# Kernel tuning notes

Measured on AMD Instinct MI355X. Metric: run time of the kernel, lower is better.

## Reference

```python
import jax, jax.numpy as jnp
import numpy as np

K = 3          # kernel_size
STRIDE = 1
PAD = 1
DIL = 1
K2 = K * K


def conv2d(x, w, b):
    # standard NCHW conv matching nn.Conv2d(stride, padding, dilation)
    y = jax.lax.conv_general_dilated(
        x, w, window_strides=(STRIDE, STRIDE),
        padding=[(PAD, PAD), (PAD, PAD)], rhs_dilation=(DIL, DIL),
        dimension_numbers=('NCHW', 'OIHW', 'NCHW'))
    return y + b[None, :, None, None]


def setup_inputs() -> dict:
    key = jax.random.key(0)
    ks = jax.random.split(key, 7)
    B, C, H, W, O = 4, 64, 128, 128, 64
    x = jax.random.normal(ks[0], (B, C, H, W), jnp.float32)
    weight = jax.random.normal(ks[1], (O, C, K, K), jnp.float32) * 0.05
    bias = jax.random.normal(ks[2], (O,), jnp.float32) * 0.05
    # offset/modulation convs (small weights so sample points stay near grid)
    offset_w = jax.random.normal(ks[3], (2 * K2, C, K, K), jnp.float32) * 0.01
    offset_b = jax.random.normal(ks[4], (2 * K2,), jnp.float32) * 0.1
    mod_w = jax.random.normal(ks[5], (K2, C, K, K), jnp.float32) * 0.01
    mod_b = jnp.ones((K2,), jnp.float32)  # torch init: modulation bias = 1
    return dict(x=x, weight=weight, bias=bias, offset_w=offset_w,
                offset_b=offset_b, mod_w=mod_w, mod_b=mod_b)


def _forward(x, weight, bias, offset_w, offset_b, mod_w, mod_b):
    B, C, H, W = x.shape
    O = weight.shape[0]
    offsets = conv2d(x, offset_w, offset_b)              # (B, 2*K2, Ho, Wo)
    mod = jax.nn.sigmoid(conv2d(x, mod_w, mod_b))        # (B, K2, Ho, Wo)
    Ho, Wo = offsets.shape[2], offsets.shape[3]
    off = offsets.reshape(B, 2, K2, Ho, Wo)
    # base sampling position: single center per output pixel (as in source)
    base_y = jnp.arange(Ho, dtype=x.dtype) * STRIDE - PAD + (K // 2) * DIL
    base_x = jnp.arange(Wo, dtype=x.dtype) * STRIDE - PAD + (K // 2) * DIL
    sy = base_y[None, None, :, None] + off[:, 0]         # (B, K2, Ho, Wo)
    sx = base_x[None, None, None, :] + off[:, 1]
    # bilinear sampling, zero padding, align_corners=True semantics
    y0 = jnp.floor(sy)
    x0 = jnp.floor(sx)
    wy1 = sy - y0
    wx1 = sx - x0
    y0i = y0.astype(jnp.int32)
    x0i = x0.astype(jnp.int32)
    P = K2 * Ho * Wo
    xf = x.reshape(B, C, H * W)

    def gather(yi, xi):
        valid = ((yi >= 0) & (yi < H) & (xi >= 0) & (xi < W))
        lin = (jnp.clip(yi, 0, H - 1) * W + jnp.clip(xi, 0, W - 1)).reshape(B, P)
        g = jax.vmap(lambda xb, lb: xb[:, lb])(xf, lin)   # (B, C, P)
        return g * valid.reshape(B, 1, P).astype(x.dtype)

    wy1f = wy1.reshape(B, 1, P)
    wx1f = wx1.reshape(B, 1, P)
    g00 = gather(y0i, x0i)
    g01 = gather(y0i, x0i + 1)
    g10 = gather(y0i + 1, x0i)
    g11 = gather(y0i + 1, x0i + 1)
    sampled = ((1.0 - wy1f) * ((1.0 - wx1f) * g00 + wx1f * g01)
               + wy1f * ((1.0 - wx1f) * g10 + wx1f * g11))
    sampled = sampled.reshape(B, C, K2, Ho * Wo)
    wk = weight.reshape(O, C, K2)
    out = jnp.einsum('bckp,ock->bop', sampled, wk).reshape(B, O, Ho, Wo)
    out = out * mod.mean(axis=1, keepdims=True) + bias[None, :, None, None]
    return out


def reference(x, weight, bias, offset_w, offset_b, mod_w, mod_b):
    return _forward(x, weight, bias, offset_w, offset_b, mod_w, mod_b)
```

## Files before the change

kernel.cpp:

```cpp
#include <hip/hip_runtime.h>
#include <math.h>

namespace {

constexpr int B = 4, C = 64, O = 64, H = 128, W = 128, K2 = 9;
constexpr int HW = H * W;
constexpr int PIX = 128;
constexpr int STR = 64;
constexpr int WROWS = 4, WCOLS = STR + 3, WCELLS = WROWS * WCOLS;

typedef __attribute__((ext_vector_type(8))) short short8v;
typedef __attribute__((ext_vector_type(4))) float f32x4;
typedef __attribute__((ext_vector_type(2))) float f32x2;
typedef __attribute__((ext_vector_type(4))) unsigned u32x4;

__device__ __forceinline__ unsigned f2bf(float f) {
    unsigned u = __float_as_uint(f);
    return (u + 0x7FFFu + ((u >> 16) & 1u)) >> 16;
}
__device__ __forceinline__ unsigned cvtpk(float lo, float hi) {
    unsigned r;
    asm("v_cvt_pk_bf16_f32 %0, %1, %2" : "=v"(r) : "v"(lo), "v"(hi));
    return r;
}
__device__ __forceinline__ f32x2 up2(unsigned d) {
    f32x2 r;
    r[0] = __uint_as_float(d << 16);
    r[1] = __uint_as_float(d & 0xffff0000u);
    return r;
}
__device__ __forceinline__ int swz(int r, int off) {
    return (r << 7) + (off ^ ((r & 7) << 4));
}

constexpr size_t WSW_OFF = 0;
constexpr size_t WSA_OFF = 73728;
constexpr size_t WS_NEED = 110592;

__global__ void k0_pack(const float* __restrict__ w, const float* __restrict__ ow,
                        const float* __restrict__ mw, unsigned char* __restrict__ ws)
{
    const int id = blockIdx.x * 256 + threadIdx.x;
    if (id < 4608) {
        const int k = id >> 9, rem = id & 511, ks = rem >> 8, r2 = rem & 255;
        const int ot = r2 >> 6, lane = r2 & 63;
        const int o = ot * 16 + (lane & 15), cb = ks * 32 + (lane >> 4) * 8;
        unsigned pk[4];
        #pragma unroll
        for (int e = 0; e < 4; ++e)
            pk[e] = f2bf(w[(o * C + cb + 2 * e) * 9 + k])
                  | (f2bf(w[(o * C + cb + 2 * e + 1) * 9 + k]) << 16);
        *(uint4*)(ws + WSW_OFF + (size_t)id * 16) = make_uint4(pk[0], pk[1], pk[2], pk[3]);
    } else if (id < 6912) {
        const int id2 = id - 4608;
        const int k = id2 >> 8, rem = id2 & 255, ks = rem >> 7, r2 = rem & 127;
        const int mt = r2 >> 6, lane = r2 & 63;
        const int r = mt * 16 + (lane & 15), cb = ks * 32 + (lane >> 4) * 8;
        unsigned pk[4];
        #pragma unroll
        for (int e = 0; e < 4; ++e) {
            float v0 = 0.f, v1 = 0.f;
            const int c0 = cb + 2 * e;
            if (r < 18)      { v0 = ow[(r * C + c0) * 9 + k];        v1 = ow[(r * C + c0 + 1) * 9 + k]; }
            else if (r < 27) { v0 = mw[((r - 18) * C + c0) * 9 + k]; v1 = mw[((r - 18) * C + c0 + 1) * 9 + k]; }
            pk[e] = f2bf(v0) | (f2bf(v1) << 16);
        }
        *(uint4*)(ws + WSA_OFF + (size_t)id2 * 16) = make_uint4(pk[0], pk[1], pk[2], pk[3]);
    }
}

__global__ __launch_bounds__(256, 3)
void dcn_fused14(const float* __restrict__ x, const float* __restrict__ bias,
                 const float* __restrict__ ob, const float* __restrict__ mb,
                 const unsigned char* __restrict__ ws, float* __restrict__ out)
{
    __shared__ __align__(16) unsigned char sW[WCELLS * 128];
    __shared__ float offL[18 * STR];

    const int tid = threadIdx.x;
    const int lane = tid & 63, wv = tid >> 6;
    const int lrow = lane & 15, lk = lane >> 4;

    const int raw = blockIdx.x;
    const int bid = (raw & 7) * 128 + (raw >> 3);
    const int b = bid >> 8;
    const int s = bid & 255;
    const int ho = s >> 1;
    const int wo0 = (s & 1) * STR;

    const float* __restrict__ xb = x + b * C * HW;

    for (int t = tid; t < 2 * WCELLS; t += 256) {
        const int cell = t >> 1, chalf = t & 1;
        const int row = cell / WCOLS, col = cell - row * WCOLS;
        const int y = ho - 1 + row, xg = wo0 - 2 + col;
        const bool v = (y >= 0) & (y < H) & (xg >= 0) & (xg < W);
        const float vf = v ? 1.f : 0.f;
        const float* __restrict__ xp = xb + (v ? (y * W + xg) : 0);
        #pragma unroll
        for (int q = 0; q < 4; ++q) {
            unsigned pk[4];
            #pragma unroll
            for (int e = 0; e < 4; ++e) {
                const int c0 = chalf * 32 + q * 8 + 2 * e;
                pk[e] = cvtpk(vf * xp[c0 * HW], vf * xp[(c0 + 1) * HW]);
            }
            *(uint4*)(sW + swz(cell, chalf * 64 + q * 16)) = make_uint4(pk[0], pk[1], pk[2], pk[3]);
        }
    }
    __syncthreads();

    f32x4 oacc[2];
    #pragma unroll
    for (int mt = 0; mt < 2; ++mt)
        #pragma unroll
        for (int j = 0; j < 4; ++j) oacc[mt][j] = 0.f;

    #pragma unroll
    for (int k = 0; k < 9; ++k) {
        const int ky = k / 3, kx = k - ky * 3;
        const int cellb = ky * WCOLS + (wv * 16 + lrow) + kx + 1;
        #pragma unroll
        for (int ks = 0; ks < 2; ++ks) {
            short8v bf = *(const short8v*)(sW + swz(cellb, ks * 64 + lk * 16));
            #pragma unroll
            for (int mt = 0; mt < 2; ++mt) {
                short8v af = *(const short8v*)(ws + WSA_OFF +
                    (size_t)((((k * 2 + ks) * 2 + mt) * 64 + lane)) * 16);
                oacc[mt] = __builtin_amdgcn_mfma_f32_16x16x32_bf16(af, bf, oacc[mt], 0, 0, 0);
            }
        }
    }

    float mpart = 0.f;
    {
        const int pc = wv * 16 + lrow;
        #pragma unroll
        for (int mt = 0; mt < 2; ++mt) {
            #pragma unroll
            for (int j = 0; j < 4; ++j) {
                const int r = mt * 16 + lk * 4 + j;
                const float val = oacc[mt][j];
                if (r < 9)       offL[r * STR + pc] = (float)ho + ob[r] + val;
                else if (r < 18) offL[r * STR + pc] = (float)(wo0 + pc) + ob[r] + val;
                else if (r < 27) mpart += 1.f / (1.f + __expf(-(val + mb[r - 18])));
            }
        }
    }
    mpart += __shfl_xor(mpart, 16);
    mpart += __shfl_xor(mpart, 32);
    const float mm = mpart * (1.f / 9.f);
    __syncthreads();

    const int px = wv * 16 + lrow;

    float syr[9], sxr[9];
    #pragma unroll
    for (int k = 0; k < 9; ++k) {
        syr[k] = offL[k * STR + px];
        sxr[k] = offL[(9 + k) * STR + px];
    }

    f32x4 acc[4];
    #pragma unroll
    for (int ot = 0; ot < 4; ++ot)
        #pragma unroll
        for (int j = 0; j < 4; ++j) acc[ot][j] = 0.f;

    short8v afq[8], afn[8];
    #pragma unroll
    for (int i = 0; i < 8; ++i)
        afq[i] = *(const short8v*)(ws + WSW_OFF + (size_t)(i * 64 + lane) * 16);

    #pragma unroll
    for (int k = 0; k < 9; ++k) {
        const float syv = syr[k];
        const float sxv = sxr[k];
        const float fy = floorf(syv), fx = floorf(sxv);
        const float wy1 = syv - fy, wx1 = sxv - fx;
        const float wy0 = 1.f - wy1, wx0 = 1.f - wx1;
        const int y0 = (int)fy, x0 = (int)fx;
        const int rw = y0 - (ho - 1), cw = x0 - (wo0 - 2);
        const bool inw = (rw >= 0) & (rw <= WROWS - 2) & (cw >= 0) & (cw <= WCOLS - 2);
        const float u00 = wy0 * wx0, u01 = wy0 * wx1;
        const float u10 = wy1 * wx0, u11 = wy1 * wx1;

        short8v bfrag[2];
        if (__builtin_expect(inw, 1)) {
            const int c00 = rw * WCOLS + cw;
            #pragma unroll
            for (int ks = 0; ks < 2; ++ks) {
                const int chOff = ks * 64 + lk * 16;
                const uint4 d00 = *(const uint4*)(sW + swz(c00,             chOff));
                const uint4 d01 = *(const uint4*)(sW + swz(c00 + 1,         chOff));
                const uint4 d10 = *(const uint4*)(sW + swz(c00 + WCOLS,     chOff));
                const uint4 d11 = *(const uint4*)(sW + swz(c00 + WCOLS + 1, chOff));
                auto bil = [&](unsigned a, unsigned bb, unsigned c, unsigned d) -> unsigned {
                    f32x2 sacc = up2(a);
                    sacc *= u00;
                    sacc += up2(bb) * u01;
                    sacc += up2(c)  * u10;
                    sacc += up2(d)  * u11;
                    return cvtpk(sacc[0], sacc[1]);
                };
                u32x4 wvv;
                wvv[0] = bil(d00.x, d01.x, d10.x, d11.x);
                wvv[1] = bil(d00.y, d01.y, d10.y, d11.y);
                wvv[2] = bil(d00.z, d01.z, d10.z, d11.z);
                wvv[3] = bil(d00.w, d01.w, d10.w, d11.w);
                bfrag[ks] = __builtin_bit_cast(short8v, wvv);
            }
        } else {
            const float vy0 = (y0 >= 0 && y0 < H) ? 1.f : 0.f;
            const float vy1 = (y0 + 1 >= 0 && y0 + 1 < H) ? 1.f : 0.f;
            const float vx0 = (x0 >= 0 && x0 < W) ? 1.f : 0.f;
            const float vx1 = (x0 + 1 >= 0 && x0 + 1 < W) ? 1.f : 0.f;
            const int cy0 = min(max(y0, 0), H - 1), cy1 = min(max(y0 + 1, 0), H - 1);
            const int cx0 = min(max(x0, 0), W - 1), cx1 = min(max(x0 + 1, 0), W - 1);
            const int l00 = cy0 * W + cx0, l01 = cy0 * W + cx1;
            const int l10 = cy1 * W + cx0, l11 = cy1 * W + cx1;
            const float g00 = u00 * vy0 * vx0, g01 = u01 * vy0 * vx1;
            const float g10 = u10 * vy1 * vx0, g11 = u11 * vy1 * vx1;
            #pragma unroll
            for (int ks = 0; ks < 2; ++ks) {
                #pragma unroll
                for (int j = 0; j < 8; ++j) {
                    const float* __restrict__ xc = xb + (ks * 32 + lk * 8 + j) * HW;
                    const float sv = g00 * xc[l00] + g01 * xc[l01]
                                   + g10 * xc[l10] + g11 * xc[l11];
                    bfrag[ks][j] = (short)f2bf(sv);
                }
            }
        }

        if (k < 8) {
            #pragma unroll
            for (int i = 0; i < 8; ++i)
                afn[i] = *(const short8v*)(ws + WSW_OFF +
                    (size_t)(((k + 1) * 8 + i) * 64 + lane) * 16);
        }

        #pragma unroll
        for (int i = 0; i < 8; ++i)
            acc[i & 3] = __builtin_amdgcn_mfma_f32_16x16x32_bf16(
                afq[i], bfrag[i >> 2], acc[i & 3], 0, 0, 0);

        if (k < 8) {
            #pragma unroll
            for (int i = 0; i < 8; ++i) afq[i] = afn[i];
        }
    }

    #pragma unroll
    for (int ot = 0; ot < 4; ++ot) {
        #pragma unroll
        for (int j = 0; j < 4; ++j) {
            const int o = ot * 16 + lk * 4 + j;
            out[(b * O + o) * HW + ho * W + wo0 + px] = acc[ot][j] * mm + bias[o];
        }
    }
}

__global__ __launch_bounds__(256, 2)
void dcn_fallback(const float* __restrict__ x, const float* __restrict__ weight,
                  const float* __restrict__ bias, const float* __restrict__ ow,
                  const float* __restrict__ ob, const float* __restrict__ mw,
                  const float* __restrict__ mb, float* __restrict__ out)
{
    __shared__ __align__(16) unsigned char sT[PIX * 128];
    __shared__ float offL[32 * PIX];
    __shared__ float mmL[PIX];

    const int tid = threadIdx.x;
    const int lane = tid & 63;
    const int wv = tid >> 6;
    const int bid = (blockIdx.x & 7) * 64 + (blockIdx.x >> 3);
    const int b = bid >> 7;
    const int ho = bid & 127;
    const float* __restrict__ xb = x + (size_t)b * C * HW;
    const int p = tid & 127, half = tid >> 7, wo = p;
    const int lrow = lane & 15, lk = lane >> 4;

    f32x4 oacc[2][2];
    #pragma unroll
    for (int mt = 0; mt < 2; ++mt)
        #pragma unroll
        for (int nt = 0; nt < 2; ++nt)
            #pragma unroll
            for (int j = 0; j < 4; ++j) oacc[mt][nt][j] = 0.0f;

    #pragma unroll
    for (int k = 0; k < K2; ++k) {
        const int ky = k / 3, kx = k % 3;
        short8v afrA[2][2];
        #pragma unroll
        for (int ks = 0; ks < 2; ++ks)
            #pragma unroll
            for (int mt = 0; mt < 2; ++mt) {
                const int r = mt * 16 + lrow, cb = ks * 32 + lk * 8;
                #pragma unroll
                for (int j = 0; j < 8; ++j) {
                    float wvv = 0.0f;
                    if (r < 18)      wvv = ow[((size_t)(r * C + cb + j)) * 9 + k];
                    else if (r < 27) wvv = mw[((size_t)((r - 18) * C + cb + j)) * 9 + k];
                    afrA[ks][mt][j] = (short)f2bf(wvv);
                }
            }
        {
            const int y = ho - 1 + ky, xx = wo - 1 + kx;
            const bool v = (y >= 0) & (y < H) & (xx >= 0) & (xx < W);
            const float vf = v ? 1.0f : 0.0f;
            const float* __restrict__ xp = xb + (v ? (y * W + xx) : 0);
            #pragma unroll
            for (int q = 0; q < 4; ++q) {
                unsigned pk[4];
                #pragma unroll
                for (int e = 0; e < 4; ++e) {
                    const int c0 = half * 32 + q * 8 + e * 2;
                    pk[e] = f2bf(vf * xp[(size_t)c0 * HW]) | (f2bf(vf * xp[(size_t)(c0 + 1) * HW]) << 16);
                }
                *(uint4*)(sT + swz(p, half * 64 + q * 16)) = make_uint4(pk[0], pk[1], pk[2], pk[3]);
            }
        }
        __syncthreads();
        #pragma unroll
        for (int ks = 0; ks < 2; ++ks)
            #pragma unroll
            for (int nt = 0; nt < 2; ++nt) {
                const int pc = wv * 32 + nt * 16 + lrow;
                short8v bfr = *(const short8v*)(sT + swz(pc, ks * 64 + lk * 16));
                #pragma unroll
                for (int mt = 0; mt < 2; ++mt)
                    oacc[mt][nt] = __builtin_amdgcn_mfma_f32_16x16x32_bf16(afrA[ks][mt], bfr, oacc[mt][nt], 0, 0, 0);
            }
        __syncthreads();
    }

    #pragma unroll
    for (int mt = 0; mt < 2; ++mt)
        #pragma unroll
        for (int nt = 0; nt < 2; ++nt)
            #pragma unroll
            for (int j = 0; j < 4; ++j) {
                const int r = mt * 16 + lk * 4 + j;
                const int pc = wv * 32 + nt * 16 + lrow;
                float bv = 0.0f;
                if (r < 18)      bv = ob[r];
                else if (r < 27) bv = mb[r - 18];
                offL[r * PIX + pc] = oacc[mt][nt][j] + bv;
            }
    __syncthreads();

    float sy[K2], sx[K2];
    #pragma unroll
    for (int k = 0; k < K2; ++k) {
        sy[k] = (float)ho + offL[k * PIX + p];
        sx[k] = (float)wo + offL[(9 + k) * PIX + p];
    }
    if (half == 0) {
        float mm = 0.0f;
        #pragma unroll
        for (int k = 0; k < K2; ++k)
            mm += 1.0f / (1.0f + __expf(-offL[(18 + k) * PIX + p]));
        mmL[p] = mm * (1.0f / 9.0f);
    }

    f32x4 acc[8];
    #pragma unroll
    for (int nt = 0; nt < 8; ++nt)
        #pragma unroll
        for (int j = 0; j < 4; ++j) acc[nt][j] = 0.0f;

    #pragma unroll
    for (int k = 0; k < K2; ++k) {
        short8v afr[2];
        #pragma unroll
        for (int ks = 0; ks < 2; ++ks) {
            const int o = wv * 16 + lrow, cb = ks * 32 + lk * 8;
            #pragma unroll
            for (int j = 0; j < 8; ++j)
                afr[ks][j] = (short)f2bf(weight[((size_t)(o * C + cb + j)) * 9 + k]);
        }
        {
            const float fy = floorf(sy[k]), fx = floorf(sx[k]);
            const float wy1 = sy[k] - fy, wx1 = sx[k] - fx;
            const float wy0 = 1.0f - wy1, wx0 = 1.0f - wx1;
            const int y0 = (int)fy, x0 = (int)fx, y1 = y0 + 1, x1 = x0 + 1;
            const float vy0 = (y0 >= 0 && y0 < H) ? 1.0f : 0.0f;
            const float vy1 = (y1 >= 0 && y1 < H) ? 1.0f : 0.0f;
            const float vx0 = (x0 >= 0 && x0 < W) ? 1.0f : 0.0f;
            const float vx1 = (x1 >= 0 && x1 < W) ? 1.0f : 0.0f;
            const int cy0 = min(max(y0, 0), H - 1), cy1 = min(max(y1, 0), H - 1);
            const int cx0 = min(max(x0, 0), W - 1), cx1 = min(max(x1, 0), W - 1);
            const int l00 = cy0 * W + cx0, l01 = cy0 * W + cx1;
            const int l10 = cy1 * W + cx0, l11 = cy1 * W + cx1;
            const float w00 = wy0 * wx0 * vy0 * vx0, w01 = wy0 * wx1 * vy0 * vx1;
            const float w10 = wy1 * wx0 * vy1 * vx0, w11 = wy1 * wx1 * vy1 * vx1;
            #pragma unroll
            for (int q = 0; q < 4; ++q) {
                unsigned pk[4];
                #pragma unroll
                for (int e = 0; e < 4; ++e) {
                    const int c0 = half * 32 + q * 8 + e * 2;
                    const float* __restrict__ xc0 = xb + (size_t)c0 * HW;
                    const float* __restrict__ xc1 = xc0 + HW;
                    const float s0 = w00 * xc0[l00] + w01 * xc0[l01] + w10 * xc0[l10] + w11 * xc0[l11];
                    const float s1 = w00 * xc1[l00] + w01 * xc1[l01] + w10 * xc1[l10] + w11 * xc1[l11];
                    pk[e] = f2bf(s0) | (f2bf(s1) << 16);
                }
                *(uint4*)(sT + swz(p, half * 64 + q * 16)) = make_uint4(pk[0], pk[1], pk[2], pk[3]);
            }
        }
        __syncthreads();
        #pragma unroll
        for (int ks = 0; ks < 2; ++ks)
            #pragma unroll
            for (int nt = 0; nt < 8; ++nt) {
                const int pc = nt * 16 + lrow;
                short8v bfr = *(const short8v*)(sT + swz(pc, ks * 64 + lk * 16));
                acc[nt] = __builtin_amdgcn_mfma_f32_16x16x32_bf16(afr[ks], bfr, acc[nt], 0, 0, 0);
            }
        __syncthreads();
    }

    float bv[4];
    #pragma unroll
    for (int j = 0; j < 4; ++j) bv[j] = bias[wv * 16 + lk * 4 + j];
    #pragma unroll
    for (int nt = 0; nt < 8; ++nt) {
        const int pc = nt * 16 + lrow;
        const float mmv = mmL[pc];
        #pragma unroll
        for (int j = 0; j < 4; ++j) {
            const int o = wv * 16 + lk * 4 + j;
            out[((size_t)(b * O + o)) * HW + ho * W + pc] = acc[nt][j] * mmv + bv[j];
        }
    }
}

}

extern "C" void kernel_launch(void* const* d_in, const int* in_sizes, int n_in,
                              void* d_out, int out_size, void* d_ws, size_t ws_size,
                              hipStream_t stream)
{
    const float* x  = (const float*)d_in[0];
    const float* w  = (const float*)d_in[1];
    const float* bs = (const float*)d_in[2];
    const float* ow = (const float*)d_in[3];
    const float* ob = (const float*)d_in[4];
    const float* mw = (const float*)d_in[5];
    const float* mb = (const float*)d_in[6];
    float* out = (float*)d_out;

    if (ws_size < WS_NEED) {
        dim3 grid(B * H), block(256);
        hipLaunchKernelGGL(dcn_fallback, grid, block, 0, stream,
                           x, w, bs, ow, ob, mw, mb, out);
        return;
    }

    unsigned char* ws = (unsigned char*)d_ws;
    hipLaunchKernelGGL(k0_pack, dim3(27), dim3(256), 0, stream, w, ow, mw, ws);
    hipLaunchKernelGGL(dcn_fused14, dim3(1024), dim3(256), 0, stream,
                       x, bs, ob, mb, (const unsigned char*)ws, out);
}
```

Baseline: 41.11 us.

## Process two output rows per block to share input window and weight fragments

Each block now covers two output rows instead of one. It loads a 5-row input window into LDS and reuses the main-conv weight fragments for both rows, then launches half as many blocks. The intent is to cut redundant global reads of the input halo and of the weights. In exchange it doubles the accumulator registers per thread and uses more LDS, which may lower occupancy under the 3-blocks-per-SIMD launch bound. With 512 blocks the grid gives the chip fewer waves to schedule.

```diff
diff --git a/kernel.cpp b/kernel.cpp
--- a/kernel.cpp
+++ b/kernel.cpp
@@ -7,7 +7,7 @@
 constexpr int HW = H * W;
 constexpr int PIX = 128;
 constexpr int STR = 64;
-constexpr int WROWS = 4, WCOLS = STR + 3, WCELLS = WROWS * WCOLS;
+constexpr int WROWS = 5, WCOLS = STR + 3, WCELLS = WROWS * WCOLS;
 
 typedef __attribute__((ext_vector_type(8))) short short8v;
 typedef __attribute__((ext_vector_type(4))) float f32x4;
@@ -70,30 +70,30 @@
 }
 
 __global__ __launch_bounds__(256, 3)
-void dcn_fused14(const float* __restrict__ x, const float* __restrict__ bias,
+void dcn_fused15(const float* __restrict__ x, const float* __restrict__ bias,
                  const float* __restrict__ ob, const float* __restrict__ mb,
                  const unsigned char* __restrict__ ws, float* __restrict__ out)
 {
     __shared__ __align__(16) unsigned char sW[WCELLS * 128];
-    __shared__ float offL[18 * STR];
+    __shared__ float offL[2 * 18 * STR];
 
     const int tid = threadIdx.x;
     const int lane = tid & 63, wv = tid >> 6;
     const int lrow = lane & 15, lk = lane >> 4;
 
     const int raw = blockIdx.x;
-    const int bid = (raw & 7) * 128 + (raw >> 3);
-    const int b = bid >> 8;
-    const int s = bid & 255;
-    const int ho = s >> 1;
-    const int wo0 = (s & 1) * STR;
+    const int bid = (raw & 7) * 64 + (raw >> 3);
+    const int b = bid >> 7;
+    const int r2_ = bid & 127;
+    const int ho0 = (r2_ >> 1) << 1;
+    const int wo0 = (r2_ & 1) << 6;
 
     const float* __restrict__ xb = x + b * C * HW;
 
     for (int t = tid; t < 2 * WCELLS; t += 256) {
         const int cell = t >> 1, chalf = t & 1;
         const int row = cell / WCOLS, col = cell - row * WCOLS;
-        const int y = ho - 1 + row, xg = wo0 - 2 + col;
+        const int y = ho0 - 1 + row, xg = wo0 - 2 + col;
         const bool v = (y >= 0) & (y < H) & (xg >= 0) & (xg < W);
         const float vf = v ? 1.f : 0.f;
         const float* __restrict__ xp = xb + (v ? (y * W + xg) : 0);
@@ -110,62 +110,61 @@
     }
     __syncthreads();
 
-    f32x4 oacc[2];
-    #pragma unroll
-    for (int mt = 0; mt < 2; ++mt)
-        #pragma unroll
-        for (int j = 0; j < 4; ++j) oacc[mt][j] = 0.f;
-
-    #pragma unroll
-    for (int k = 0; k < 9; ++k) {
-        const int ky = k / 3, kx = k - ky * 3;
-        const int cellb = ky * WCOLS + (wv * 16 + lrow) + kx + 1;
-        #pragma unroll
-        for (int ks = 0; ks < 2; ++ks) {
-            short8v bf = *(const short8v*)(sW + swz(cellb, ks * 64 + lk * 16));
+    float mmr[2];
+    #pragma unroll
+    for (int rr = 0; rr < 2; ++rr) {
+        f32x4 oacc[2];
+        #pragma unroll
+        for (int mt = 0; mt < 2; ++mt)
+            #pragma unroll
+            for (int j = 0; j < 4; ++j) oacc[mt][j] = 0.f;
+
+        #pragma unroll
+        for (int k = 0; k < 9; ++k) {
+            const int ky = k / 3, kx = k - ky * 3;
+            const int cellb = (rr + ky) * WCOLS + (wv * 16 + lrow) + kx + 1;
+            #pragma unroll
+            for (int ks = 0; ks < 2; ++ks) {
+                short8v bf = *(const short8v*)(sW + swz(cellb, ks * 64 + lk * 16));
+                #pragma unroll
+                for (int mt = 0; mt < 2; ++mt) {
+                    short8v af = *(const short8v*)(ws + WSA_OFF +
+                        (size_t)((((k * 2 + ks) * 2 + mt) * 64 + lane)) * 16);
+                    oacc[mt] = __builtin_amdgcn_mfma_f32_16x16x32_bf16(af, bf, oacc[mt], 0, 0, 0);
+                }
+            }
+        }
+
+        float mpart = 0.f;
+        {
+            const int pc = wv * 16 + lrow;
             #pragma unroll
             for (int mt = 0; mt < 2; ++mt) {
-                short8v af = *(const short8v*)(ws + WSA_OFF +
-                    (size_t)((((k * 2 + ks) * 2 + mt) * 64 + lane)) * 16);
-                oacc[mt] = __builtin_amdgcn_mfma_f32_16x16x32_bf16(af, bf, oacc[mt], 0, 0, 0);
-            }
-        }
-    }
-
-    float mpart = 0.f;
-    {
-        const int pc = wv * 16 + lrow;
-        #pragma unroll
-        for (int mt = 0; mt < 2; ++mt) {
-            #pragma unroll
-            for (int j = 0; j < 4; ++j) {
-                const int r = mt * 16 + lk * 4 + j;
-                const float val = oacc[mt][j];
-                if (r < 9)       offL[r * STR + pc] = (float)ho + ob[r] + val;
-                else if (r < 18) offL[r * STR + pc] = (float)(wo0 + pc) + ob[r] + val;
-                else if (r < 27) mpart += 1.f / (1.f + __expf(-(val + mb[r - 18])));
-            }
-        }
-    }
-    mpart += __shfl_xor(mpart, 16);
-    mpart += __shfl_xor(mpart, 32);
-    const float mm = mpart * (1.f / 9.f);
+                #pragma unroll
+                for (int j = 0; j < 4; ++j) {
+                    const int r = mt * 16 + lk * 4 + j;
+                    const float val = oacc[mt][j];
+                    if (r < 9)       offL[(rr * 18 + r) * STR + pc] = (float)(ho0 + rr) + ob[r] + val;
+                    else if (r < 18) offL[(rr * 18 + r) * STR + pc] = (float)(wo0 + pc) + ob[r] + val;
+                    else if (r < 27) mpart += 1.f / (1.f + __expf(-(val + mb[r - 18])));
+                }
+            }
+        }
+        mpart += __shfl_xor(mpart, 16);
+        mpart += __shfl_xor(mpart, 32);
+        mmr[rr] = mpart * (1.f / 9.f);
+    }
     __syncthreads();
 
     const int px = wv * 16 + lrow;
 
-    float syr[9], sxr[9];
-    #pragma unroll
-    for (int k = 0; k < 9; ++k) {
-        syr[k] = offL[k * STR + px];
-        sxr[k] = offL[(9 + k) * STR + px];
-    }
-
-    f32x4 acc[4];
-    #pragma unroll
-    for (int ot = 0; ot < 4; ++ot)
-        #pragma unroll
-        for (int j = 0; j < 4; ++j) acc[ot][j] = 0.f;
+    f32x4 acc[2][4];
+    #pragma unroll
+    for (int rr = 0; rr < 2; ++rr)
+        #pragma unroll
+        for (int ot = 0; ot < 4; ++ot)
+            #pragma unroll
+            for (int j = 0; j < 4; ++j) acc[rr][ot][j] = 0.f;
 
     short8v afq[8], afn[8];
     #pragma unroll
@@ -174,65 +173,6 @@
 
     #pragma unroll
     for (int k = 0; k < 9; ++k) {
-        const float syv = syr[k];
-        const float sxv = sxr[k];
-        const float fy = floorf(syv), fx = floorf(sxv);
-        const float wy1 = syv - fy, wx1 = sxv - fx;
-        const float wy0 = 1.f - wy1, wx0 = 1.f - wx1;
-        const int y0 = (int)fy, x0 = (int)fx;
-        const int rw = y0 - (ho - 1), cw = x0 - (wo0 - 2);
-        const bool inw = (rw >= 0) & (rw <= WROWS - 2) & (cw >= 0) & (cw <= WCOLS - 2);
-        const float u00 = wy0 * wx0, u01 = wy0 * wx1;
-        const float u10 = wy1 * wx0, u11 = wy1 * wx1;
-
-        short8v bfrag[2];
-        if (__builtin_expect(inw, 1)) {
-            const int c00 = rw * WCOLS + cw;
-            #pragma unroll
-            for (int ks = 0; ks < 2; ++ks) {
-                const int chOff = ks * 64 + lk * 16;
-                const uint4 d00 = *(const uint4*)(sW + swz(c00,             chOff));
-                const uint4 d01 = *(const uint4*)(sW + swz(c00 + 1,         chOff));
-                const uint4 d10 = *(const uint4*)(sW + swz(c00 + WCOLS,     chOff));
-                const uint4 d11 = *(const uint4*)(sW + swz(c00 + WCOLS + 1, chOff));
-                auto bil = [&](unsigned a, unsigned bb, unsigned c, unsigned d) -> unsigned {
-                    f32x2 sacc = up2(a);
-                    sacc *= u00;
-                    sacc += up2(bb) * u01;
-                    sacc += up2(c)  * u10;
-                    sacc += up2(d)  * u11;
-                    return cvtpk(sacc[0], sacc[1]);
-                };
-                u32x4 wvv;
-                wvv[0] = bil(d00.x, d01.x, d10.x, d11.x);
-                wvv[1] = bil(d00.y, d01.y, d10.y, d11.y);
-                wvv[2] = bil(d00.z, d01.z, d10.z, d11.z);
-                wvv[3] = bil(d00.w, d01.w, d10.w, d11.w);
-                bfrag[ks] = __builtin_bit_cast(short8v, wvv);
-            }
-        } else {
-            const float vy0 = (y0 >= 0 && y0 < H) ? 1.f : 0.f;
-            const float vy1 = (y0 + 1 >= 0 && y0 + 1 < H) ? 1.f : 0.f;
-            const float vx0 = (x0 >= 0 && x0 < W) ? 1.f : 0.f;
-            const float vx1 = (x0 + 1 >= 0 && x0 + 1 < W) ? 1.f : 0.f;
-            const int cy0 = min(max(y0, 0), H - 1), cy1 = min(max(y0 + 1, 0), H - 1);
-            const int cx0 = min(max(x0, 0), W - 1), cx1 = min(max(x0 + 1, 0), W - 1);
-            const int l00 = cy0 * W + cx0, l01 = cy0 * W + cx1;
-            const int l10 = cy1 * W + cx0, l11 = cy1 * W + cx1;
-            const float g00 = u00 * vy0 * vx0, g01 = u01 * vy0 * vx1;
-            const float g10 = u10 * vy1 * vx0, g11 = u11 * vy1 * vx1;
-            #pragma unroll
-            for (int ks = 0; ks < 2; ++ks) {
-                #pragma unroll
-                for (int j = 0; j < 8; ++j) {
-                    const float* __restrict__ xc = xb + (ks * 32 + lk * 8 + j) * HW;
-                    const float sv = g00 * xc[l00] + g01 * xc[l01]
-                                   + g10 * xc[l10] + g11 * xc[l11];
-                    bfrag[ks][j] = (short)f2bf(sv);
-                }
-            }
-        }
-
         if (k < 8) {
             #pragma unroll
             for (int i = 0; i < 8; ++i)
@@ -241,9 +181,71 @@
         }
 
         #pragma unroll
-        for (int i = 0; i < 8; ++i)
-            acc[i & 3] = __builtin_amdgcn_mfma_f32_16x16x32_bf16(
-                afq[i], bfrag[i >> 2], acc[i & 3], 0, 0, 0);
+        for (int rr = 0; rr < 2; ++rr) {
+            const float syv = offL[(rr * 18 + k) * STR + px];
+            const float sxv = offL[(rr * 18 + 9 + k) * STR + px];
+            const float fy = floorf(syv), fx = floorf(sxv);
+            const float wy1 = syv - fy, wx1 = sxv - fx;
+            const float wy0 = 1.f - wy1, wx0 = 1.f - wx1;
+            const int y0 = (int)fy, x0 = (int)fx;
+            const int wrow = y0 - (ho0 - 1), cw = x0 - (wo0 - 2);
+            const bool inw = (wrow >= 0) & (wrow <= WROWS - 2) & (cw >= 0) & (cw <= WCOLS - 2);
+            const float u00 = wy0 * wx0, u01 = wy0 * wx1;
+            const float u10 = wy1 * wx0, u11 = wy1 * wx1;
+
+            short8v bfrag[2];
+            if (__builtin_expect(inw, 1)) {
+                const int c00 = wrow * WCOLS + cw;
+                #pragma unroll
+                for (int ks = 0; ks < 2; ++ks) {
+                    const int chOff = ks * 64 + lk * 16;
+                    const uint4 d00 = *(const uint4*)(sW + swz(c00,             chOff));
+                    const uint4 d01 = *(const uint4*)(sW + swz(c00 + 1,         chOff));
+                    const uint4 d10 = *(const uint4*)(sW + swz(c00 + WCOLS,     chOff));
+                    const uint4 d11 = *(const uint4*)(sW + swz(c00 + WCOLS + 1, chOff));
+                    auto bil = [&](unsigned a, unsigned bb, unsigned c, unsigned d) -> unsigned {
+                        f32x2 sacc = up2(a);
+                        sacc *= u00;
+                        sacc += up2(bb) * u01;
+                        sacc += up2(c)  * u10;
+                        sacc += up2(d)  * u11;
+                        return cvtpk(sacc[0], sacc[1]);
+                    };
+                    u32x4 wvv;
+                    wvv[0] = bil(d00.x, d01.x, d10.x, d11.x);
+                    wvv[1] = bil(d00.y, d01.y, d10.y, d11.y);
+                    wvv[2] = bil(d00.z, d01.z, d10.z, d11.z);
+                    wvv[3] = bil(d00.w, d01.w, d10.w, d11.w);
+                    bfrag[ks] = __builtin_bit_cast(short8v, wvv);
+                }
+            } else {
+                const float vy0 = (y0 >= 0 && y0 < H) ? 1.f : 0.f;
+                const float vy1 = (y0 + 1 >= 0 && y0 + 1 < H) ? 1.f : 0.f;
+                const float vx0 = (x0 >= 0 && x0 < W) ? 1.f : 0.f;
+                const float vx1 = (x0 + 1 >= 0 && x0 + 1 < W) ? 1.f : 0.f;
+                const int cy0 = min(max(y0, 0), H - 1), cy1 = min(max(y0 + 1, 0), H - 1);
+                const int cx0 = min(max(x0, 0), W - 1), cx1 = min(max(x0 + 1, 0), W - 1);
+                const int l00 = cy0 * W + cx0, l01 = cy0 * W + cx1;
+                const int l10 = cy1 * W + cx0, l11 = cy1 * W + cx1;
+                const float g00 = u00 * vy0 * vx0, g01 = u01 * vy0 * vx1;
+                const float g10 = u10 * vy1 * vx0, g11 = u11 * vy1 * vx1;
+                #pragma unroll
+                for (int ks = 0; ks < 2; ++ks) {
+                    #pragma unroll
+                    for (int j = 0; j < 8; ++j) {
+                        const float* __restrict__ xc = xb + (ks * 32 + lk * 8 + j) * HW;
+                        const float sv = g00 * xc[l00] + g01 * xc[l01]
+                                       + g10 * xc[l10] + g11 * xc[l11];
+                        bfrag[ks][j] = (short)f2bf(sv);
+                    }
+                }
+            }
+
+            #pragma unroll
+            for (int i = 0; i < 8; ++i)
+                acc[rr][i & 3] = __builtin_amdgcn_mfma_f32_16x16x32_bf16(
+                    afq[i], bfrag[i >> 2], acc[rr][i & 3], 0, 0, 0);
+        }
 
         if (k < 8) {
             #pragma unroll
@@ -252,11 +254,15 @@
     }
 
     #pragma unroll
-    for (int ot = 0; ot < 4; ++ot) {
-        #pragma unroll
-        for (int j = 0; j < 4; ++j) {
-            const int o = ot * 16 + lk * 4 + j;
-            out[(b * O + o) * HW + ho * W + wo0 + px] = acc[ot][j] * mm + bias[o];
+    for (int rr = 0; rr < 2; ++rr) {
+        #pragma unroll
+        for (int ot = 0; ot < 4; ++ot) {
+            #pragma unroll
+            for (int j = 0; j < 4; ++j) {
+                const int o = ot * 16 + lk * 4 + j;
+                out[(b * O + o) * HW + (ho0 + rr) * W + wo0 + px] =
+                    acc[rr][ot][j] * mmr[rr] + bias[o];
+            }
         }
     }
 }
@@ -462,6 +468,6 @@
 
     unsigned char* ws = (unsigned char*)d_ws;
     hipLaunchKernelGGL(k0_pack, dim3(27), dim3(256), 0, stream, w, ow, mw, ws);
-    hipLaunchKernelGGL(dcn_fused14, dim3(1024), dim3(256), 0, stream,
+    hipLaunchKernelGGL(dcn_fused15, dim3(512), dim3(256), 0, stream,
                        x, bs, ob, mb, (const unsigned char*)ws, out);
 }
```

Result: slower. 48.86 us (+18.8%).
